# Performance work log

Measured on AMD Instinct MI355X. Metric: run time of the kernel, lower is better.

The kernel has to match this reference:

```python
import jax, jax.numpy as jnp
import numpy as np

NUM_HEADS = 24
EPS = 1e-6


def rms_norm(x, scale):
    # fp32 RMSNorm over last dim, matching torch F.rms_norm(eps=1e-6)
    xf = x.astype(jnp.float32)
    rrms = jax.lax.rsqrt(jnp.mean(xf * xf, axis=-1, keepdims=True) + EPS)
    return (xf * rrms * scale.astype(jnp.float32)).astype(x.dtype)


def rope_rotate(x, pe):
    # x: [B,H,L,D]; pe: [B,1,L,D/2,2,2] rotation matrices
    B, H, L, D = x.shape
    xr = x.astype(jnp.float32).reshape(B, H, L, D // 2, 1, 2)
    out = pe[..., 0] * xr[..., 0] + pe[..., 1] * xr[..., 1]  # [B,H,L,D/2,2]
    return out.reshape(B, H, L, D).astype(x.dtype)


def setup_inputs() -> dict:
    key = jax.random.key(0)
    ks = jax.random.split(key, 6)
    B, L, C = 1, 2048, 3072
    H = NUM_HEADS
    D = C // H
    x = jax.random.normal(ks[0], (B, L, C), dtype=jnp.float32)
    # pe: proper RoPE rotation matrices [[cos,-sin],[sin,cos]] -> [B,1,L,D/2,2,2]
    theta = jax.random.uniform(ks[1], (B, 1, L, D // 2), dtype=jnp.float32) * (2.0 * np.pi)
    cos, sin = jnp.cos(theta), jnp.sin(theta)
    row0 = jnp.stack([cos, -sin], axis=-1)
    row1 = jnp.stack([sin, cos], axis=-1)
    pe = jnp.stack([row0, row1], axis=-2)  # [B,1,L,D/2,2,2]
    w_qkv = jax.random.normal(ks[2], (3 * C, C), dtype=jnp.float32) * (1.0 / np.sqrt(C))
    q_scale = jnp.ones((D,), dtype=jnp.float32)
    k_scale = jnp.ones((D,), dtype=jnp.float32)
    w_proj = jax.random.normal(ks[3], (C, C), dtype=jnp.float32) * (1.0 / np.sqrt(C))
    b_proj = jnp.zeros((C,), dtype=jnp.float32)
    return {"x": x, "pe": pe, "w_qkv": w_qkv, "q_scale": q_scale,
            "k_scale": k_scale, "w_proj": w_proj, "b_proj": b_proj}


def reference(x, pe, w_qkv, q_scale, k_scale, w_proj, b_proj):
    B, L, C = x.shape
    H = NUM_HEADS
    D = C // H
    qkv = x @ w_qkv.T                                   # [B,L,3C]
    qkv = qkv.reshape(B, L, 3, H, D).transpose(2, 0, 3, 1, 4)  # [3,B,H,L,D]
    q, k, v = qkv[0], qkv[1], qkv[2]
    q = rms_norm(q, q_scale)
    k = rms_norm(k, k_scale)
    q = rope_rotate(q, pe)
    k = rope_rotate(k, pe)
    scale = 1.0 / np.sqrt(D)
    scores = jnp.einsum('bhqd,bhkd->bhqk', q, k) * jnp.asarray(scale, q.dtype)
    attn = jax.nn.softmax(scores, axis=-1)
    out = jnp.einsum('bhqk,bhkd->bhqd', attn, v)        # [B,H,L,D]
    out = out.transpose(0, 2, 1, 3).reshape(B, L, C)    # [B,L,C]
    return out @ w_proj.T + b_proj
```

## Files before the change

kernel.cpp:

```cpp
#include <hip/hip_runtime.h>

typedef __attribute__((ext_vector_type(8))) __bf16 bf16x8;
typedef __attribute__((ext_vector_type(4))) float f32x4;

typedef __attribute__((address_space(1))) void gvoid;
typedef __attribute__((address_space(3))) void lvoid;

__device__ __forceinline__ float bf2f(unsigned int u) {
    union { unsigned int u; float f; } v; v.u = u << 16; return v.f;
}
__device__ __forceinline__ unsigned short f2bf(float f) {
    union { float f; unsigned int u; } v; v.f = f;
    unsigned int r = v.u + 0x7fffu + ((v.u >> 16) & 1u);
    return (unsigned short)(r >> 16);
}
__device__ __forceinline__ unsigned int pack2(float a, float b) {
    return (unsigned int)f2bf(a) | ((unsigned int)f2bf(b) << 16);
}
__device__ __forceinline__ void async16(const void* g, void* l) {
    __builtin_amdgcn_global_load_lds((gvoid*)g, (lvoid*)l, 16, 0, 0);
}
__device__ __forceinline__ float exp2f_hw(float x) {
    return __builtin_amdgcn_exp2f(x);
}


__global__ __launch_bounds__(256)
void cvt_bf16(const float4* __restrict__ s, uint4* __restrict__ d, int n8) {
    int i = blockIdx.x * 256 + threadIdx.x;
    if (i >= n8) return;
    float4 a = s[2 * i], b = s[2 * i + 1];
    uint4 o;
    o.x = pack2(a.x, a.y); o.y = pack2(a.z, a.w);
    o.z = pack2(b.x, b.y); o.w = pack2(b.z, b.w);
    d[i] = o;
}

#define GEMM_CORE(A_, lda_, B_, ldb_, K_)                                        \
    __shared__ __align__(16) unsigned short As[4][4096];                         \
    __shared__ __align__(16) unsigned short Bs[4][4096];                         \
    const int t = threadIdx.x, lane = t & 63;                                    \
    const int wm = t >> 7, wn = (t >> 6) & 1;                                    \
    const int lr = lane & 15, kc = lane >> 4;                                    \
    const int NK = (K_) / 32;                                                    \
    const int e0 = t * 8, e1 = (256 + t) * 8;                                    \
    const int r0 = e0 >> 5, c0 = (e0 >> 3) & 3;                                  \
    const int r1 = e1 >> 5, c1 = (e1 >> 3) & 3;                                  \
    const int g0 = (c0 ^ ((r0 >> 1) & 3)) * 8;                                   \
    const int g1 = (c1 ^ ((r1 >> 1) & 3)) * 8;                                   \
    const unsigned short* Ag0 = &(A_)[(size_t)(m0 + r0) * (lda_) + g0];          \
    const unsigned short* Ag1 = &(A_)[(size_t)(m0 + r1) * (lda_) + g1];          \
    const unsigned short* Bg0 = &(B_)[(size_t)(n0 + r0) * (ldb_) + g0];          \
    const unsigned short* Bg1 = &(B_)[(size_t)(n0 + r1) * (ldb_) + g1];          \
    f32x4 acc[4][4] = {};                                                        \
    RSTAGE(0) RSTAGE(1) RSTAGE(2)                                                \
    asm volatile("s_waitcnt vmcnt(8)" ::: "memory");                             \
    __builtin_amdgcn_s_barrier();                                                \
    for (int kt = 0; kt < NK; ++kt) {                                            \
        const int sl = kt & 3;                                                   \
        bf16x8 af[4], bfr[4];                                                    \
        _Pragma("unroll")                                                        \
        for (int i = 0; i < 4; ++i) {                                            \
            int ra = wm * 64 + i * 16 + lr;                                      \
            int rb = wn * 64 + i * 16 + lr;                                      \
            af[i]  = *(const bf16x8*)&As[sl][ra * 32 + ((kc ^ ((ra >> 1) & 3)) * 8)]; \
            bfr[i] = *(const bf16x8*)&Bs[sl][rb * 32 + ((kc ^ ((rb >> 1) & 3)) * 8)]; \
        }                                                                        \
        if (kt + 3 < NK) RSTAGE(kt + 3)                                          \
        asm volatile("s_waitcnt lgkmcnt(0)" ::: "memory");                       \
        __builtin_amdgcn_sched_barrier(0);                                       \
        __builtin_amdgcn_s_setprio(1);                                           \
        _Pragma("unroll")                                                        \
        for (int mi = 0; mi < 4; ++mi)                                           \
            _Pragma("unroll")                                                    \
            for (int ni = 0; ni < 4; ++ni)                                       \
                acc[mi][ni] = __builtin_amdgcn_mfma_f32_16x16x32_bf16(           \
                    af[mi], bfr[ni], acc[mi][ni], 0, 0, 0);                      \
        __builtin_amdgcn_s_setprio(0);                                           \
        if (kt + 3 < NK)      { asm volatile("s_waitcnt vmcnt(8)" ::: "memory"); } \
        else if (kt + 2 < NK) { asm volatile("s_waitcnt vmcnt(4)" ::: "memory"); } \
        else if (kt + 1 < NK) { asm volatile("s_waitcnt vmcnt(0)" ::: "memory"); } \
        __builtin_amdgcn_s_barrier();                                            \
    }

#define RSTAGE(kt_) { const int s_ = (kt_) & 3; const size_t k_ = (size_t)(kt_) * 32; \
        async16(Ag0 + k_, &As[s_][e0]); async16(Ag1 + k_, &As[s_][e1]);               \
        async16(Bg0 + k_, &Bs[s_][e0]); async16(Bg1 + k_, &Bs[s_][e1]); }

__global__ __launch_bounds__(256, 2)
void gemm_qkv(const unsigned short* __restrict__ A, const unsigned short* __restrict__ B,
              unsigned short* __restrict__ qk, unsigned short* __restrict__ vt) {
    const int n0 = blockIdx.x * 128, m0 = blockIdx.y * 128;
    GEMM_CORE(A, 3072, B, 3072, 3072)
    const int rb0 = kc * 4;
#pragma unroll
    for (int mi = 0; mi < 4; ++mi)
#pragma unroll
        for (int ni = 0; ni < 4; ++ni) {
            int col = n0 + wn * 64 + ni * 16 + lr;
#pragma unroll
            for (int r = 0; r < 4; ++r) {
                int row = m0 + wm * 64 + mi * 16 + rb0 + r;
                unsigned short v = f2bf(acc[mi][ni][r]);
                if (col < 6144) qk[(size_t)row * 6144 + col] = v;
                else            vt[(size_t)(col - 6144) * 2048 + row] = v;
            }
        }
}

__global__ __launch_bounds__(256, 2)
void gemm_proj(const unsigned short* __restrict__ A, const unsigned short* __restrict__ B,
               const float* __restrict__ bias, float* __restrict__ out) {
    const int n0 = blockIdx.x * 128, m0 = blockIdx.y * 128;
    GEMM_CORE(A, 6144, B, 3072, 3072)
    const int rb0 = kc * 4;
#pragma unroll
    for (int mi = 0; mi < 4; ++mi)
#pragma unroll
        for (int ni = 0; ni < 4; ++ni) {
            int col = n0 + wn * 64 + ni * 16 + lr;
            float badd = bias[col];
#pragma unroll
            for (int r = 0; r < 4; ++r) {
                int row = m0 + wm * 64 + mi * 16 + rb0 + r;
                out[(size_t)row * 3072 + col] = acc[mi][ni][r] + badd;
            }
        }
}

__global__ __launch_bounds__(256)
void attn2(unsigned short* __restrict__ qk, const unsigned short* __restrict__ vt) {
    __shared__ __align__(16) unsigned short Ks[64 * 128];
    __shared__ __align__(16) unsigned short Vs[128 * 64];
    __shared__ __align__(16) unsigned short Ps[4 * 16 * 64];
    const int t = threadIdx.x, lane = t & 63, w = t >> 6;
    const int h = blockIdx.x, qblk = blockIdx.y * 64;
    const int lr = lane & 15, kc = lane >> 4;
    const float sc2 = 0.08838834764831845f * 1.4426950408889634f;

    bf16x8 aq[4];
#pragma unroll
    for (int ks = 0; ks < 4; ++ks)
        aq[ks] = *(const bf16x8*)&qk[(size_t)(qblk + w * 16 + lr) * 6144 + h * 128 + ks * 32 + kc * 8];

    f32x4 o[8] = {};
    float mst[4], lst[4];
#pragma unroll
    for (int r = 0; r < 4; ++r) { mst[r] = -1e30f; lst[r] = 0.0f; }

    unsigned short* Pw = &Ps[w * 1024];

#pragma unroll
    for (int i = 0; i < 4; ++i) {
        int e = (i * 256 + t) * 8;
        {
            int row = e >> 7, c8 = (e >> 3) & 15;
            int gc = (c8 ^ (row & 15)) * 8;
            async16(&qk[(size_t)row * 6144 + 3072 + h * 128 + gc], &Ks[e]);
        }
        {
            int row = e >> 6, c8 = (e >> 3) & 7;
            int gc = (c8 ^ (row & 7)) * 8;
            async16(&vt[(size_t)(h * 128 + row) * 2048 + gc], &Vs[e]);
        }
    }

    for (int kb = 0; kb < 2048; kb += 64) {
        __syncthreads();

        bf16x8 pk[4], pv[4];
        const bool pf = (kb + 64) < 2048;
        if (pf) {
#pragma unroll
            for (int i = 0; i < 4; ++i) {
                int e = (i * 256 + t) * 8;
                {   int row = e >> 7, c8 = (e >> 3) & 15;
                    int gc = (c8 ^ (row & 15)) * 8;
                    pk[i] = *(const bf16x8*)&qk[(size_t)(kb + 64 + row) * 6144 + 3072 + h * 128 + gc];
                }
                {   int row = e >> 6, c8 = (e >> 3) & 7;
                    int gc = (c8 ^ (row & 7)) * 8;
                    pv[i] = *(const bf16x8*)&vt[(size_t)(h * 128 + row) * 2048 + kb + 64 + gc];
                }
            }
        }

        f32x4 s[4] = {};
#pragma unroll
        for (int nt = 0; nt < 4; ++nt) {
            int rk = nt * 16 + lr;
#pragma unroll
            for (int ks = 0; ks < 4; ++ks) {
                int ck = ks * 4 + kc;
                bf16x8 bk = *(const bf16x8*)&Ks[rk * 128 + ((ck ^ (rk & 15)) * 8)];
                s[nt] = __builtin_amdgcn_mfma_f32_16x16x32_bf16(aq[ks], bk, s[nt], 0, 0, 0);
            }
        }

#pragma unroll
        for (int r = 0; r < 4; ++r) {
            float vmax = fmaxf(fmaxf(s[0][r], s[1][r]), fmaxf(s[2][r], s[3][r]));
#pragma unroll
            for (int off = 8; off >= 1; off >>= 1) vmax = fmaxf(vmax, __shfl_xor(vmax, off));
            float mn = fmaxf(mst[r], vmax);
            float al = exp2f_hw((mst[r] - mn) * sc2);
            mst[r] = mn;
            float ps = 0.0f;
#pragma unroll
            for (int nt = 0; nt < 4; ++nt) {
                float p = exp2f_hw((s[nt][r] - mn) * sc2);
                s[nt][r] = p;
                ps += p;
            }
#pragma unroll
            for (int off = 8; off >= 1; off >>= 1) ps += __shfl_xor(ps, off);
            lst[r] = lst[r] * al + ps;
#pragma unroll
            for (int dt = 0; dt < 8; ++dt) o[dt][r] *= al;
        }

#pragma unroll
        for (int nt = 0; nt < 4; ++nt) {
            int col = nt * 16 + lr;
            int chunk = col >> 3, cin = col & 7;
#pragma unroll
            for (int r = 0; r < 4; ++r) {
                int q = kc * 4 + r;
                Pw[q * 64 + ((chunk ^ (q & 7)) * 8 + cin)] = f2bf(s[nt][r]);
            }
        }

#pragma unroll
        for (int ks2 = 0; ks2 < 2; ++ks2) {
            int ck = ks2 * 4 + kc;
            bf16x8 ap = *(const bf16x8*)&Pw[lr * 64 + ((ck ^ (lr & 7)) * 8)];
#pragma unroll
            for (int dt = 0; dt < 8; ++dt) {
                int rv = dt * 16 + lr;
                bf16x8 bv = *(const bf16x8*)&Vs[rv * 64 + ((ck ^ (rv & 7)) * 8)];
                o[dt] = __builtin_amdgcn_mfma_f32_16x16x32_bf16(ap, bv, o[dt], 0, 0, 0);
            }
        }
        __syncthreads();

        if (pf) {
#pragma unroll
            for (int i = 0; i < 4; ++i) {
                int e = (i * 256 + t) * 8;
                *(bf16x8*)&Ks[e] = pk[i];
                *(bf16x8*)&Vs[e] = pv[i];
            }
        }
    }

#pragma unroll
    for (int dt = 0; dt < 8; ++dt)
#pragma unroll
        for (int r = 0; r < 4; ++r) {
            int row = qblk + w * 16 + kc * 4 + r;
            qk[(size_t)row * 6144 + h * 128 + dt * 16 + lr] = f2bf(o[dt][r] / lst[r]);
        }
}


__global__ __launch_bounds__(256)
void norm_rope(unsigned short* __restrict__ qk, const float* __restrict__ pe,
               const float* __restrict__ q_scale, const float* __restrict__ k_scale) {
    const int wid = threadIdx.x >> 6, lane = threadIdx.x & 63;
    int pid = blockIdx.x * 4 + wid;
    const int isK = pid >= 49152;
    int p2 = isK ? pid - 49152 : pid;
    const int h = p2 >> 11, l = p2 & 2047;

    unsigned short* src = qk + (size_t)l * 6144 + (isK ? 3072 : 0) + h * 128 + lane * 2;
    unsigned int xu = *(const unsigned int*)src;
    float x0 = bf2f(xu & 0xffffu), x1 = bf2f(xu >> 16);
    float ss = x0 * x0 + x1 * x1;
#pragma unroll
    for (int off = 32; off >= 1; off >>= 1) ss += __shfl_xor(ss, off);
    float rr = rsqrtf(ss * (1.0f / 128.0f) + 1e-6f);

    const float* sc = isK ? k_scale : q_scale;
    float2 s2 = *(const float2*)(sc + lane * 2);
    float y0 = x0 * rr * s2.x;
    float y1 = x1 * rr * s2.y;

    float4 p4 = *(const float4*)(pe + ((size_t)l * 64 + lane) * 4);
    float o0 = p4.x * y0 + p4.y * y1;
    float o1 = p4.z * y0 + p4.w * y1;

    *(unsigned int*)src = pack2(o0, o1);
}


template <bool A32, bool B32, bool C32, bool HAS_BIAS, bool TRANS_C>
__global__ __launch_bounds__(256, 2)
void gemm_bt(const void* __restrict__ Ap, const void* __restrict__ Bp,
             const float* __restrict__ bias, void* __restrict__ Cp,
             int M, int N, int K, int lda, int ldc) {
    __shared__ __align__(16) unsigned short As[128 * 40];
    __shared__ __align__(16) unsigned short Bs[128 * 40];
    const int t = threadIdx.x, lane = t & 63;
    const int wm = t >> 7, wn = (t >> 6) & 1;
    const int m0 = blockIdx.x * 128, n0 = blockIdx.y * 128;
    const int lr = lane & 15, kc = lane >> 4;
    f32x4 acc[4][4] = {};

    for (int k0 = 0; k0 < K; k0 += 32) {
        float4 ra32[4], rb32[4];
        bf16x8 ra16[2], rb16[2];
        if constexpr (A32) {
            const float* A = (const float*)Ap;
#pragma unroll
            for (int i = 0; i < 4; ++i) {
                int idx = i * 256 + t, row = idx >> 3, c4 = idx & 7;
                ra32[i] = *(const float4*)&A[(size_t)(m0 + row) * lda + k0 + c4 * 4];
            }
        } else {
            const unsigned short* A = (const unsigned short*)Ap;
#pragma unroll
            for (int i = 0; i < 2; ++i) {
                int idx = i * 256 + t, row = idx >> 2, c8 = idx & 3;
                ra16[i] = *(const bf16x8*)&A[(size_t)(m0 + row) * lda + k0 + c8 * 8];
            }
        }
        if constexpr (B32) {
            const float* B = (const float*)Bp;
#pragma unroll
            for (int i = 0; i < 4; ++i) {
                int idx = i * 256 + t, row = idx >> 3, c4 = idx & 7;
                rb32[i] = *(const float4*)&B[(size_t)(n0 + row) * K + k0 + c4 * 4];
            }
        } else {
            const unsigned short* B = (const unsigned short*)Bp;
#pragma unroll
            for (int i = 0; i < 2; ++i) {
                int idx = i * 256 + t, row = idx >> 2, c8 = idx & 3;
                rb16[i] = *(const bf16x8*)&B[(size_t)(n0 + row) * K + k0 + c8 * 8];
            }
        }
        __syncthreads();
        if constexpr (A32) {
#pragma unroll
            for (int i = 0; i < 4; ++i) {
                int idx = i * 256 + t, row = idx >> 3, c4 = idx & 7;
                uint2 p = { pack2(ra32[i].x, ra32[i].y), pack2(ra32[i].z, ra32[i].w) };
                *(uint2*)&As[row * 40 + c4 * 4] = p;
            }
        } else {
#pragma unroll
            for (int i = 0; i < 2; ++i) {
                int idx = i * 256 + t, row = idx >> 2, c8 = idx & 3;
                *(bf16x8*)&As[row * 40 + c8 * 8] = ra16[i];
            }
        }
        if constexpr (B32) {
#pragma unroll
            for (int i = 0; i < 4; ++i) {
                int idx = i * 256 + t, row = idx >> 3, c4 = idx & 7;
                uint2 p = { pack2(rb32[i].x, rb32[i].y), pack2(rb32[i].z, rb32[i].w) };
                *(uint2*)&Bs[row * 40 + c4 * 4] = p;
            }
        } else {
#pragma unroll
            for (int i = 0; i < 2; ++i) {
                int idx = i * 256 + t, row = idx >> 2, c8 = idx & 3;
                *(bf16x8*)&Bs[row * 40 + c8 * 8] = rb16[i];
            }
        }
        __syncthreads();
        bf16x8 af[4], bfr[4];
#pragma unroll
        for (int i = 0; i < 4; ++i) {
            af[i]  = *(const bf16x8*)&As[(wm * 64 + i * 16 + lr) * 40 + kc * 8];
            bfr[i] = *(const bf16x8*)&Bs[(wn * 64 + i * 16 + lr) * 40 + kc * 8];
        }
#pragma unroll
        for (int mi = 0; mi < 4; ++mi)
#pragma unroll
            for (int ni = 0; ni < 4; ++ni)
                acc[mi][ni] = __builtin_amdgcn_mfma_f32_16x16x32_bf16(af[mi], bfr[ni], acc[mi][ni], 0, 0, 0);
    }
    const int rb0 = kc * 4;
#pragma unroll
    for (int mi = 0; mi < 4; ++mi) {
#pragma unroll
        for (int ni = 0; ni < 4; ++ni) {
            int col = n0 + wn * 64 + ni * 16 + lr;
            float badd = HAS_BIAS ? bias[col] : 0.0f;
#pragma unroll
            for (int r = 0; r < 4; ++r) {
                int row = m0 + wm * 64 + mi * 16 + rb0 + r;
                size_t off = TRANS_C ? ((size_t)col * ldc + row) : ((size_t)row * ldc + col);
                if (C32) ((float*)Cp)[off] = acc[mi][ni][r] + badd;
                else     ((unsigned short*)Cp)[off] = f2bf(acc[mi][ni][r] + badd);
            }
        }
    }
}

__global__ __launch_bounds__(256, 2)
void attn_slow(unsigned short* __restrict__ qk, const unsigned short* __restrict__ vt) {
    __shared__ __align__(16) unsigned short Ks[64 * 136];
    __shared__ __align__(16) unsigned short Vs[128 * 72];
    __shared__ __align__(16) unsigned short Ps[4 * 32 * 72];
    const int t = threadIdx.x, lane = t & 63, w = t >> 6;
    const int h = blockIdx.y, q0 = blockIdx.x * 128;
    const int lr = lane & 15, kc = lane >> 4;
    const float scale = 0.08838834764831845f;

    bf16x8 aq[2][4];
#pragma unroll
    for (int mf = 0; mf < 2; ++mf)
#pragma unroll
        for (int ks = 0; ks < 4; ++ks)
            aq[mf][ks] = *(const bf16x8*)&qk[(size_t)(q0 + w * 32 + mf * 16 + lr) * 6144 + h * 128 + ks * 32 + kc * 8];

    f32x4 o[2][8] = {};
    float mst[2][4], lst[2][4];
#pragma unroll
    for (int mf = 0; mf < 2; ++mf)
#pragma unroll
        for (int r = 0; r < 4; ++r) { mst[mf][r] = -1e30f; lst[mf][r] = 0.0f; }

    unsigned short* Pw = &Ps[w * 32 * 72];

    for (int kb = 0; kb < 2048; kb += 64) {
        bf16x8 rk[4], rv[4];
#pragma unroll
        for (int i = 0; i < 4; ++i) {
            int idx = i * 256 + t;
            { int row = idx >> 4, c8 = idx & 15;
              rk[i] = *(const bf16x8*)&qk[(size_t)(kb + row) * 6144 + 3072 + h * 128 + c8 * 8]; }
            { int row = idx >> 3, c8 = idx & 7;
              rv[i] = *(const bf16x8*)&vt[(size_t)(h * 128 + row) * 2048 + kb + c8 * 8]; }
        }
        __syncthreads();
#pragma unroll
        for (int i = 0; i < 4; ++i) {
            int idx = i * 256 + t;
            { int row = idx >> 4, c8 = idx & 15; *(bf16x8*)&Ks[row * 136 + c8 * 8] = rk[i]; }
            { int row = idx >> 3, c8 = idx & 7;  *(bf16x8*)&Vs[row * 72 + c8 * 8] = rv[i]; }
        }
        __syncthreads();

        f32x4 s[2][4] = {};
#pragma unroll
        for (int nt = 0; nt < 4; ++nt) {
            int rkr = nt * 16 + lr;
#pragma unroll
            for (int ks = 0; ks < 4; ++ks) {
                bf16x8 bk = *(const bf16x8*)&Ks[rkr * 136 + (ks * 4 + kc) * 8];
#pragma unroll
                for (int mf = 0; mf < 2; ++mf)
                    s[mf][nt] = __builtin_amdgcn_mfma_f32_16x16x32_bf16(aq[mf][ks], bk, s[mf][nt], 0, 0, 0);
            }
        }
#pragma unroll
        for (int mf = 0; mf < 2; ++mf)
#pragma unroll
            for (int nt = 0; nt < 4; ++nt)
#pragma unroll
                for (int r = 0; r < 4; ++r) s[mf][nt][r] *= scale;

#pragma unroll
        for (int mf = 0; mf < 2; ++mf) {
#pragma unroll
            for (int r = 0; r < 4; ++r) {
                float vmax = fmaxf(fmaxf(s[mf][0][r], s[mf][1][r]), fmaxf(s[mf][2][r], s[mf][3][r]));
#pragma unroll
                for (int off = 8; off >= 1; off >>= 1) vmax = fmaxf(vmax, __shfl_xor(vmax, off));
                float mn = fmaxf(mst[mf][r], vmax);
                float al = __expf(mst[mf][r] - mn);
                mst[mf][r] = mn;
                float ps = 0.0f;
#pragma unroll
                for (int nt = 0; nt < 4; ++nt) {
                    float p = __expf(s[mf][nt][r] - mn);
                    s[mf][nt][r] = p;
                    ps += p;
                }
#pragma unroll
                for (int off = 8; off >= 1; off >>= 1) ps += __shfl_xor(ps, off);
                lst[mf][r] = lst[mf][r] * al + ps;
#pragma unroll
                for (int dt = 0; dt < 8; ++dt) o[mf][dt][r] *= al;
            }
        }

#pragma unroll
        for (int mf = 0; mf < 2; ++mf)
#pragma unroll
            for (int nt = 0; nt < 4; ++nt)
#pragma unroll
                for (int r = 0; r < 4; ++r)
                    Pw[(mf * 16 + kc * 4 + r) * 72 + nt * 16 + lr] = f2bf(s[mf][nt][r]);

#pragma unroll
        for (int ks2 = 0; ks2 < 2; ++ks2) {
            bf16x8 ap[2];
#pragma unroll
            for (int mf = 0; mf < 2; ++mf)
                ap[mf] = *(const bf16x8*)&Pw[(mf * 16 + lr) * 72 + (ks2 * 4 + kc) * 8];
#pragma unroll
            for (int dt = 0; dt < 8; ++dt) {
                bf16x8 bv = *(const bf16x8*)&Vs[(dt * 16 + lr) * 72 + (ks2 * 4 + kc) * 8];
#pragma unroll
                for (int mf = 0; mf < 2; ++mf)
                    o[mf][dt] = __builtin_amdgcn_mfma_f32_16x16x32_bf16(ap[mf], bv, o[mf][dt], 0, 0, 0);
            }
        }
        __syncthreads();
    }

#pragma unroll
    for (int mf = 0; mf < 2; ++mf)
#pragma unroll
        for (int dt = 0; dt < 8; ++dt)
#pragma unroll
            for (int r = 0; r < 4; ++r) {
                int row = q0 + w * 32 + mf * 16 + kc * 4 + r;
                qk[(size_t)row * 6144 + h * 128 + dt * 16 + lr] = f2bf(o[mf][dt][r] / lst[mf][r]);
            }
}

__global__ void fill_two(float* p, int n) {
    int i = blockIdx.x * 256 + threadIdx.x;
    if (i < n) p[i] = 2.0f;
}

extern "C" void kernel_launch(void* const* d_in, const int* in_sizes, int n_in,
                              void* d_out, int out_size, void* d_ws, size_t ws_size,
                              hipStream_t stream) {
    const float* x       = (const float*)d_in[0];
    const float* pe      = (const float*)d_in[1];
    const float* w_qkv   = (const float*)d_in[2];
    const float* q_scale = (const float*)d_in[3];
    const float* k_scale = (const float*)d_in[4];
    const float* w_proj  = (const float*)d_in[5];
    const float* b_proj  = (const float*)d_in[6];
    float* out = (float*)d_out;

    if (ws_size >= 125829120ull) {
        unsigned short* ws     = (unsigned short*)d_ws;
        unsigned short* xb     = ws;
        unsigned short* wqkvb  = ws + 6291456;
        unsigned short* wprojb = ws + 34603008;
        unsigned short* qk     = ws + 44040192;
        unsigned short* vt     = ws + 56623104;

        cvt_bf16<<<3072, 256, 0, stream>>>((const float4*)x, (uint4*)xb, 786432);
        cvt_bf16<<<13824, 256, 0, stream>>>((const float4*)w_qkv, (uint4*)wqkvb, 3538944);
        cvt_bf16<<<4608, 256, 0, stream>>>((const float4*)w_proj, (uint4*)wprojb, 1179648);

        gemm_qkv<<<dim3(72, 16), 256, 0, stream>>>(xb, wqkvb, qk, vt);
        norm_rope<<<24576, 256, 0, stream>>>(qk, pe, q_scale, k_scale);
        attn2<<<dim3(24, 32), 256, 0, stream>>>(qk, vt);
        gemm_proj<<<dim3(24, 16), 256, 0, stream>>>(qk, wprojb, b_proj, out);
        return;
    }

    if (ws_size < 37748736ull) {
        fill_two<<<(6291456 + 255) / 256, 256, 0, stream>>>(out, 6291456);
        return;
    }

    unsigned short* qk = (unsigned short*)d_ws;
    unsigned short* vt = qk + 12582912;

    gemm_bt<true, true, false, false, false><<<dim3(16, 48), 256, 0, stream>>>(
        x, w_qkv, nullptr, qk, 2048, 6144, 3072, 3072, 6144);
    norm_rope<<<24576, 256, 0, stream>>>(qk, pe, q_scale, k_scale);
    gemm_bt<true, true, false, false, true><<<dim3(16, 24), 256, 0, stream>>>(
        x, w_qkv + (size_t)6144 * 3072, nullptr, vt, 2048, 3072, 3072, 3072, 2048);
    attn_slow<<<dim3(16, 24), 256, 0, stream>>>(qk, vt);
    gemm_bt<false, true, true, true, false><<<dim3(16, 24), 256, 0, stream>>>(
        qk, w_proj, b_proj, out, 2048, 3072, 3072, 6144, 3072);
}
```

Before: 599.3 us.

## Enlarge QKV GEMM tile to 128x256 with 3-stage LDS pipeline

The QKV projection GEMM now uses a 128x256 output tile per block instead of 128x128. Each of the four waves computes a 128x64 slice with 8x4 MFMA accumulators, so every A fragment is reused across more B columns. The LDS ring drops from four stages to three to fit the larger B tile, and the grid halves to 36x16 blocks. The aim is to raise arithmetic intensity and cut redundant A loads, at the cost of more accumulator registers (risking occupancy under launch_bounds 2), fewer blocks in flight, and shallower prefetch.

```diff
diff --git a/kernel.cpp b/kernel.cpp
--- a/kernel.cpp
+++ b/kernel.cpp
@@ -90,17 +90,79 @@
 __global__ __launch_bounds__(256, 2)
 void gemm_qkv(const unsigned short* __restrict__ A, const unsigned short* __restrict__ B,
               unsigned short* __restrict__ qk, unsigned short* __restrict__ vt) {
-    const int n0 = blockIdx.x * 128, m0 = blockIdx.y * 128;
-    GEMM_CORE(A, 3072, B, 3072, 3072)
+    __shared__ __align__(16) unsigned short As[3][4096];
+    __shared__ __align__(16) unsigned short Bs[3][8192];
+    const int n0 = blockIdx.x * 256, m0 = blockIdx.y * 128;
+    const int t = threadIdx.x, lane = t & 63, w = t >> 6;
+    const int lr = lane & 15, kc = lane >> 4;
+    const int NK = 96;
+
+    const int ea0 = t * 8,         ra0 = ea0 >> 5, ca0 = (ea0 >> 3) & 3;
+    const int ea1 = (256 + t) * 8, ra1 = ea1 >> 5, ca1 = (ea1 >> 3) & 3;
+    const int ga0 = (ca0 ^ ((ra0 >> 1) & 3)) * 8;
+    const int ga1 = (ca1 ^ ((ra1 >> 1) & 3)) * 8;
+    const unsigned short* Ag0 = &A[(size_t)(m0 + ra0) * 3072 + ga0];
+    const unsigned short* Ag1 = &A[(size_t)(m0 + ra1) * 3072 + ga1];
+    int eb[4];
+    const unsigned short* Bg[4];
+#pragma unroll
+    for (int i = 0; i < 4; ++i) {
+        eb[i] = (i * 256 + t) * 8;
+        int rb = eb[i] >> 5, cb = (eb[i] >> 3) & 3;
+        int gb = (cb ^ ((rb >> 1) & 3)) * 8;
+        Bg[i] = &B[(size_t)(n0 + rb) * 3072 + gb];
+    }
+
+#define QSTAGE(kt_) { const int s_ = (kt_) % 3; const size_t k_ = (size_t)(kt_) * 32; \
+        async16(Ag0 + k_, &As[s_][ea0]); async16(Ag1 + k_, &As[s_][ea1]);             \
+        async16(Bg[0] + k_, &Bs[s_][eb[0]]); async16(Bg[1] + k_, &Bs[s_][eb[1]]);     \
+        async16(Bg[2] + k_, &Bs[s_][eb[2]]); async16(Bg[3] + k_, &Bs[s_][eb[3]]); }
+
+    f32x4 acc[8][4] = {};
+
+    QSTAGE(0) QSTAGE(1)
+    asm volatile("s_waitcnt vmcnt(6)" ::: "memory");
+    __builtin_amdgcn_s_barrier();
+
+    for (int kt = 0; kt < NK; ++kt) {
+        const int sl = kt % 3;
+        bf16x8 af[8], bfr[4];
+#pragma unroll
+        for (int i = 0; i < 8; ++i) {
+            int ra = i * 16 + lr;
+            af[i] = *(const bf16x8*)&As[sl][ra * 32 + ((kc ^ ((ra >> 1) & 3)) * 8)];
+        }
+#pragma unroll
+        for (int i = 0; i < 4; ++i) {
+            int rb = w * 64 + i * 16 + lr;
+            bfr[i] = *(const bf16x8*)&Bs[sl][rb * 32 + ((kc ^ ((rb >> 1) & 3)) * 8)];
+        }
+        if (kt + 2 < NK) QSTAGE(kt + 2)
+        asm volatile("s_waitcnt lgkmcnt(0)" ::: "memory");
+        __builtin_amdgcn_sched_barrier(0);
+        __builtin_amdgcn_s_setprio(1);
+#pragma unroll
+        for (int mi = 0; mi < 8; ++mi)
+#pragma unroll
+            for (int ni = 0; ni < 4; ++ni)
+                acc[mi][ni] = __builtin_amdgcn_mfma_f32_16x16x32_bf16(
+                    af[mi], bfr[ni], acc[mi][ni], 0, 0, 0);
+        __builtin_amdgcn_s_setprio(0);
+        if (kt + 2 < NK) { asm volatile("s_waitcnt vmcnt(6)" ::: "memory"); }
+        else             { asm volatile("s_waitcnt vmcnt(0)" ::: "memory"); }
+        __builtin_amdgcn_s_barrier();
+    }
+#undef QSTAGE
+
     const int rb0 = kc * 4;
 #pragma unroll
-    for (int mi = 0; mi < 4; ++mi)
+    for (int mi = 0; mi < 8; ++mi)
 #pragma unroll
         for (int ni = 0; ni < 4; ++ni) {
-            int col = n0 + wn * 64 + ni * 16 + lr;
+            int col = n0 + w * 64 + ni * 16 + lr;
 #pragma unroll
             for (int r = 0; r < 4; ++r) {
-                int row = m0 + wm * 64 + mi * 16 + rb0 + r;
+                int row = m0 + mi * 16 + rb0 + r;
                 unsigned short v = f2bf(acc[mi][ni][r]);
                 if (col < 6144) qk[(size_t)row * 6144 + col] = v;
                 else            vt[(size_t)(col - 6144) * 2048 + row] = v;
@@ -553,7 +615,7 @@
         cvt_bf16<<<13824, 256, 0, stream>>>((const float4*)w_qkv, (uint4*)wqkvb, 3538944);
         cvt_bf16<<<4608, 256, 0, stream>>>((const float4*)w_proj, (uint4*)wprojb, 1179648);
 
-        gemm_qkv<<<dim3(72, 16), 256, 0, stream>>>(xb, wqkvb, qk, vt);
+        gemm_qkv<<<dim3(36, 16), 256, 0, stream>>>(xb, wqkvb, qk, vt);
         norm_rope<<<24576, 256, 0, stream>>>(qk, pe, q_scale, k_scale);
         attn2<<<dim3(24, 32), 256, 0, stream>>>(qk, vt);
         gemm_proj<<<dim3(24, 16), 256, 0, stream>>>(qk, wprojb, b_proj, out);
```

Result: no change. 603.8 us (+0.7%).

## Widen QKV GEMM tile to 128x256 with direct-to-register B loads and block swizzle

Applied to the files above, without the earlier changes.

The QKV GEMM now uses 128x256 tiles. Only A is staged through LDS, double-buffered with an XOR swizzle, while each wave loads its B fragments straight from global memory into double-buffered registers. Block indices are remapped so that consecutive blocks cluster on the same N column (intended for XCD/L2 locality), and the projection GEMM gets the same remap. The aim is higher MFMA work per LDS byte and better cache reuse, at the cost of more registers (acc[4][8] plus two B buffers), which may limit occupancy.

```diff
diff --git a/kernel.cpp b/kernel.cpp
--- a/kernel.cpp
+++ b/kernel.cpp
@@ -90,14 +90,81 @@
 __global__ __launch_bounds__(256, 2)
 void gemm_qkv(const unsigned short* __restrict__ A, const unsigned short* __restrict__ B,
               unsigned short* __restrict__ qk, unsigned short* __restrict__ vt) {
-    const int n0 = blockIdx.x * 128, m0 = blockIdx.y * 128;
-    GEMM_CORE(A, 3072, B, 3072, 3072)
+    __shared__ __align__(16) unsigned short As[2][4096];
+    const int bid = blockIdx.y * 36 + blockIdx.x;
+    const int w9  = (bid & 7) * 72 + (bid >> 3);
+    const int n0 = (w9 >> 4) * 256, m0 = (w9 & 15) * 128;
+    const int t = threadIdx.x, lane = t & 63, w = t >> 6;
+    const int wm = w >> 1, wn = w & 1;
+    const int lr = lane & 15, kc = lane >> 4;
+    const int NK = 96;
+
+    const int ea0 = t * 8,         ra0 = ea0 >> 5, ca0 = (ea0 >> 3) & 3;
+    const int ea1 = (256 + t) * 8, ra1 = ea1 >> 5, ca1 = (ea1 >> 3) & 3;
+    const int ga0 = (ca0 ^ ((ra0 >> 1) & 3)) * 8;
+    const int ga1 = (ca1 ^ ((ra1 >> 1) & 3)) * 8;
+    const unsigned short* Ag0 = &A[(size_t)(m0 + ra0) * 3072 + ga0];
+    const unsigned short* Ag1 = &A[(size_t)(m0 + ra1) * 3072 + ga1];
+
+    const unsigned short* Bw = &B[(size_t)(n0 + wn * 128 + lr) * 3072 + kc * 8];
+
+#define ASTAGE(kt_) { const int s_ = (kt_) & 1; const size_t k_ = (size_t)(kt_) * 32; \
+        async16(Ag0 + k_, &As[s_][ea0]); async16(Ag1 + k_, &As[s_][ea1]); }
+#define BLOAD(dst_, kt_) { const size_t k_ = (size_t)(kt_) * 32;                      \
+        _Pragma("unroll")                                                             \
+        for (int i_ = 0; i_ < 8; ++i_)                                                \
+            dst_[i_] = *(const bf16x8*)&Bw[(size_t)i_ * 49152 + k_]; }
+
+    f32x4 acc[4][8] = {};
+    bf16x8 b0[8], b1[8];
+
+    ASTAGE(0) ASTAGE(1)
+    BLOAD(b0, 0)
+    asm volatile("s_waitcnt vmcnt(10)" ::: "memory");
+    __builtin_amdgcn_s_barrier();
+
+#define QITER(BC, BN, kt_)                                                            \
+    {                                                                                 \
+        const int sl = (kt_) & 1;                                                     \
+        bf16x8 af[4];                                                                 \
+        _Pragma("unroll")                                                             \
+        for (int i = 0; i < 4; ++i) {                                                 \
+            int ra = wm * 64 + i * 16 + lr;                                           \
+            af[i] = *(const bf16x8*)&As[sl][ra * 32 + ((kc ^ ((ra >> 1) & 3)) * 8)];  \
+        }                                                                             \
+        asm volatile("s_waitcnt lgkmcnt(0)" ::: "memory");                            \
+        __builtin_amdgcn_s_barrier();                               \
+        if ((kt_) + 2 < NK) ASTAGE((kt_) + 2)                       \
+        if ((kt_) + 1 < NK) BLOAD(BN, (kt_) + 1)                                      \
+        if ((kt_) + 2 < NK)      { asm volatile("s_waitcnt vmcnt(10)" ::: "memory"); }\
+        else if ((kt_) + 1 < NK) { asm volatile("s_waitcnt vmcnt(8)"  ::: "memory"); }\
+        else                     { asm volatile("s_waitcnt vmcnt(0)"  ::: "memory"); }\
+        __builtin_amdgcn_sched_barrier(0);                                            \
+        __builtin_amdgcn_s_setprio(1);                                                \
+        _Pragma("unroll")                                                             \
+        for (int mi = 0; mi < 4; ++mi)                                                \
+            _Pragma("unroll")                                                         \
+            for (int ni = 0; ni < 8; ++ni)                                            \
+                acc[mi][ni] = __builtin_amdgcn_mfma_f32_16x16x32_bf16(                \
+                    af[mi], BC[ni], acc[mi][ni], 0, 0, 0);                            \
+        __builtin_amdgcn_s_setprio(0);                                                \
+        __builtin_amdgcn_s_barrier();                                                 \
+    }
+
+    for (int kt = 0; kt < NK; kt += 2) {
+        QITER(b0, b1, kt)
+        QITER(b1, b0, kt + 1)
+    }
+#undef QITER
+#undef BLOAD
+#undef ASTAGE
+
     const int rb0 = kc * 4;
 #pragma unroll
     for (int mi = 0; mi < 4; ++mi)
 #pragma unroll
-        for (int ni = 0; ni < 4; ++ni) {
-            int col = n0 + wn * 64 + ni * 16 + lr;
+        for (int ni = 0; ni < 8; ++ni) {
+            int col = n0 + wn * 128 + ni * 16 + lr;
 #pragma unroll
             for (int r = 0; r < 4; ++r) {
                 int row = m0 + wm * 64 + mi * 16 + rb0 + r;
@@ -111,7 +178,9 @@
 __global__ __launch_bounds__(256, 2)
 void gemm_proj(const unsigned short* __restrict__ A, const unsigned short* __restrict__ B,
                const float* __restrict__ bias, float* __restrict__ out) {
-    const int n0 = blockIdx.x * 128, m0 = blockIdx.y * 128;
+    const int bid = blockIdx.y * 24 + blockIdx.x;
+    const int w9  = (bid & 7) * 48 + (bid >> 3);
+    const int n0 = (w9 >> 4) * 128, m0 = (w9 & 15) * 128;
     GEMM_CORE(A, 6144, B, 3072, 3072)
     const int rb0 = kc * 4;
 #pragma unroll
@@ -553,7 +622,7 @@
         cvt_bf16<<<13824, 256, 0, stream>>>((const float4*)w_qkv, (uint4*)wqkvb, 3538944);
         cvt_bf16<<<4608, 256, 0, stream>>>((const float4*)w_proj, (uint4*)wprojb, 1179648);
 
-        gemm_qkv<<<dim3(72, 16), 256, 0, stream>>>(xb, wqkvb, qk, vt);
+        gemm_qkv<<<dim3(36, 16), 256, 0, stream>>>(xb, wqkvb, qk, vt);
         norm_rope<<<24576, 256, 0, stream>>>(qk, pe, q_scale, k_scale);
         attn2<<<dim3(24, 32), 256, 0, stream>>>(qk, vt);
         gemm_proj<<<dim3(24, 16), 256, 0, stream>>>(qk, wprojb, b_proj, out);
```

After: 762.7 us. 1.27x slower.
